# Kernel optimization log

Measured on AMD Instinct MI355X. Metric: run time of the kernel, lower is better.

Reference implementation:

```python
import jax, jax.numpy as jnp
import numpy as np

IN_FEATURES = 4096
OUT_FEATURES = 32000


def setup_inputs() -> dict:
    key = jax.random.key(0)
    kx, kw, ks, kb = jax.random.split(key, 4)
    x = jax.random.normal(kx, (16, 1, IN_FEATURES), dtype=jnp.float32)
    # int8 weight buffer, per torch.randint(-128, 127, ...)
    weight_int8 = jax.random.randint(kw, (OUT_FEATURES, IN_FEATURES), -128, 127, dtype=jnp.int8)
    scale = jax.random.uniform(ks, (OUT_FEATURES, 1), dtype=jnp.float32)
    bias = jax.random.uniform(kb, (1, OUT_FEATURES), dtype=jnp.float32)
    return {"x": x, "weight_int8": weight_int8, "scale": scale, "bias": bias}


def reference(x, weight_int8, scale, bias):
    # F.linear(x, W.type_as(x)): upcast int8 weight to activation dtype, then matmul
    w = weight_int8.astype(x.dtype)               # [O, I]
    out = jnp.einsum('bsi,oi->bso', x, w)         # [B, S, O]
    out = out * scale.T                           # per-output-channel scale, [1, O] broadcast
    out = out + bias                              # [1, O] broadcast
    return out.astype(x.dtype)
```

## Files before the change

kernel.cpp:

```cpp
#include <hip/hip_runtime.h>

#define IN_F  4096
#define OUT_F 32000
#define KC    128
#define NT    (IN_F / KC)

typedef __attribute__((ext_vector_type(8))) short bf16x8;
typedef __attribute__((ext_vector_type(4))) float f32x4;
typedef unsigned int u32;

__device__ __forceinline__ short bf(float f) {
    __bf16 h = (__bf16)f;
    short s;
    __builtin_memcpy(&s, &h, 2);
    return s;
}

__device__ __forceinline__ void gload16(const void* g, void* l) {
    __builtin_amdgcn_global_load_lds(
        (const __attribute__((address_space(1))) u32*)g,
        (__attribute__((address_space(3))) u32*)l, 16, 0, 0);
}

__device__ __forceinline__ int swzW(int r) {
    return ((r & 7) << 5) | (((r >> 3) & 1) << 4);
}

__global__ __launch_bounds__(256) void w8a16_kernel(
    const int* __restrict__ W, const float* __restrict__ X,
    const float* __restrict__ scale, const float* __restrict__ bias,
    float* __restrict__ out)
{
    __shared__ __align__(16) int   Wl[2][64][KC];
    __shared__ __align__(16) short Xl[2][16][KC];

    const int tid  = threadIdx.x;
    const int lane = tid & 63;
    const int wave = tid >> 6;
    const int n    = lane & 15;
    const int kg   = lane >> 4;
    const int lo   = lane & 31;
    const int hi   = lane >> 5;
    const int o_base = blockIdx.x * 64;

    float4 xreg[2];
    f32x4  acc = {0.f, 0.f, 0.f, 0.f};

    #define LOADX(t)                                                              \
        _Pragma("unroll")                                                         \
        for (int j = 0; j < 2; ++j) {                                             \
            const int r = wave * 4 + 2 * j + hi;                                  \
            xreg[j] = *reinterpret_cast<const float4*>(                           \
                X + (size_t)r * IN_F + (t) * KC + lo * 4);                        \
        }

    #define GLOADW(buf, t)                                                        \
        _Pragma("unroll")                                                         \
        for (int j = 0; j < 8; ++j) {                                             \
            const int r  = wave * 16 + 2 * j + hi;                                \
            const char* gp = (const char*)W                                       \
                + ((size_t)(o_base + r) * IN_F + (size_t)(t) * KC) * 4            \
                + ((lo * 16) ^ swzW(r));                                          \
            gload16(gp, &Wl[buf][wave * 16 + 2 * j][0]);                          \
        }

    #define XWRITE(buf)                                                           \
        _Pragma("unroll")                                                         \
        for (int j = 0; j < 2; ++j) {                                             \
            const int r = wave * 4 + 2 * j + hi;                                  \
            short4 v;                                                             \
            v.x = bf(xreg[j].x); v.y = bf(xreg[j].y);                             \
            v.z = bf(xreg[j].z); v.w = bf(xreg[j].w);                             \
            char* p = (char*)&Xl[buf][r][0] + ((lo * 8) ^ ((r & 7) << 4));        \
            *reinterpret_cast<short4*>(p) = v;                                    \
        }

    const int rA    = wave * 16 + n;
    const int swzA  = swzW(rA);
    const int swzAx = (n & 7) << 4;

    #define COMPUTE(buf)                                                          \
        _Pragma("unroll")                                                         \
        for (int s = 0; s < KC / 32; ++s) {                                       \
            const int o0 = (s * 128 + kg * 32) ^ swzA;                            \
            const int4 qa = *reinterpret_cast<const int4*>(                       \
                (const char*)&Wl[buf][rA][0] + o0);                               \
            const int4 qb = *reinterpret_cast<const int4*>(                       \
                (const char*)&Wl[buf][rA][0] + (o0 ^ 16));                        \
            bf16x8 a;                                                             \
            a[0]=bf((float)qa.x); a[1]=bf((float)qa.y);                           \
            a[2]=bf((float)qa.z); a[3]=bf((float)qa.w);                           \
            a[4]=bf((float)qb.x); a[5]=bf((float)qb.y);                           \
            a[6]=bf((float)qb.z); a[7]=bf((float)qb.w);                           \
            const int ox = (s * 64 + kg * 16) ^ swzAx;                            \
            bf16x8 b = *reinterpret_cast<const bf16x8*>(                          \
                (const char*)&Xl[buf][n][0] + ox);                                \
            acc = __builtin_amdgcn_mfma_f32_16x16x32_bf16(a, b, acc, 0, 0, 0);    \
        }

    LOADX(0);
    GLOADW(0, 0);
    XWRITE(0);
    __syncthreads();

    for (int t = 0; t < NT; ++t) {
        const int cur = t & 1;
        if (t + 1 < NT) {
            LOADX(t + 1);
            GLOADW(cur ^ 1, t + 1);
        }
        COMPUTE(cur);
        if (t + 1 < NT) { XWRITE(cur ^ 1); }
        __syncthreads();
    }

    const int o = o_base + wave * 16 + kg * 4;
    const float4 sc = *reinterpret_cast<const float4*>(scale + o);
    const float4 bs = *reinterpret_cast<const float4*>(bias + o);
    float4 rr;
    rr.x = acc[0] * sc.x + bs.x;
    rr.y = acc[1] * sc.y + bs.y;
    rr.z = acc[2] * sc.z + bs.z;
    rr.w = acc[3] * sc.w + bs.w;
    *reinterpret_cast<float4*>(out + (size_t)n * OUT_F + o) = rr;

    #undef LOADX
    #undef GLOADW
    #undef XWRITE
    #undef COMPUTE
}

extern "C" void kernel_launch(void* const* d_in, const int* in_sizes, int n_in,
                              void* d_out, int out_size, void* d_ws, size_t ws_size,
                              hipStream_t stream) {
    const float* x     = (const float*)d_in[0];
    const int*   w     = (const int*)  d_in[1];
    const float* scale = (const float*)d_in[2];
    const float* bias  = (const float*)d_in[3];
    float* out = (float*)d_out;
    (void)in_sizes; (void)n_in; (void)d_ws; (void)ws_size; (void)out_size;

    w8a16_kernel<<<dim3(OUT_F / 64), dim3(256), 0, stream>>>(w, x, scale, bias, out);
}
```

Baseline: 98.61 us.

## Drop X LDS staging and block barriers, pipeline loads with explicit vmcnt waits

X activations are now loaded straight into per-lane registers in MFMA B-operand order and converted to bf16 there, so the shared X buffer and its write pass go away. Each wave only reads the W rows it loaded itself, so the per-tile __syncthreads is replaced by explicit s_waitcnt vmcnt/lgkmcnt and sched_barrier. The next tile's loads are issued as soon as the current LDS buffer has been read into registers, which keeps two tiles of loads in flight. In exchange, every wave redundantly fetches X from cache and register pressure goes up. Correctness also depends on the hand-counted vmcnt thresholds matching the number of issued loads.

New measurement: 108.6 us. +10.1%, slower.

```diff
diff --git a/kernel.cpp b/kernel.cpp
--- a/kernel.cpp
+++ b/kernel.cpp
@@ -31,8 +31,7 @@
     const float* __restrict__ scale, const float* __restrict__ bias,
     float* __restrict__ out)
 {
-    __shared__ __align__(16) int   Wl[2][64][KC];
-    __shared__ __align__(16) short Xl[2][16][KC];
+    __shared__ __align__(16) int Wl[2][64][KC];
 
     const int tid  = threadIdx.x;
     const int lane = tid & 63;
@@ -43,76 +42,74 @@
     const int hi   = lane >> 5;
     const int o_base = blockIdx.x * 64;
 
-    float4 xreg[2];
+    float4 xrA[8], xrB[8];
     f32x4  acc = {0.f, 0.f, 0.f, 0.f};
 
-    #define LOADX(t)                                                              \
-        _Pragma("unroll")                                                         \
-        for (int j = 0; j < 2; ++j) {                                             \
-            const int r = wave * 4 + 2 * j + hi;                                  \
-            xreg[j] = *reinterpret_cast<const float4*>(                           \
-                X + (size_t)r * IN_F + (t) * KC + lo * 4);                        \
-        }
+    const int rA   = wave * 16 + n;
+    const int swzA = swzW(rA);
 
     #define GLOADW(buf, t)                                                        \
         _Pragma("unroll")                                                         \
         for (int j = 0; j < 8; ++j) {                                             \
-            const int r  = wave * 16 + 2 * j + hi;                                \
+            const int r = wave * 16 + 2 * j + hi;                                 \
             const char* gp = (const char*)W                                       \
                 + ((size_t)(o_base + r) * IN_F + (size_t)(t) * KC) * 4            \
                 + ((lo * 16) ^ swzW(r));                                          \
             gload16(gp, &Wl[buf][wave * 16 + 2 * j][0]);                          \
         }
 
-    #define XWRITE(buf)                                                           \
+    #define LOADX(XR, t)                                                          \
         _Pragma("unroll")                                                         \
-        for (int j = 0; j < 2; ++j) {                                             \
-            const int r = wave * 4 + 2 * j + hi;                                  \
-            short4 v;                                                             \
-            v.x = bf(xreg[j].x); v.y = bf(xreg[j].y);                             \
-            v.z = bf(xreg[j].z); v.w = bf(xreg[j].w);                             \
-            char* p = (char*)&Xl[buf][r][0] + ((lo * 8) ^ ((r & 7) << 4));        \
-            *reinterpret_cast<short4*>(p) = v;                                    \
+        for (int s = 0; s < 4; ++s) {                                             \
+            const float* xp = X + (size_t)n * IN_F + (t) * KC + s * 32 + kg * 8;  \
+            XR[2*s]   = *reinterpret_cast<const float4*>(xp);                     \
+            XR[2*s+1] = *reinterpret_cast<const float4*>(xp + 4);                 \
         }
 
-    const int rA    = wave * 16 + n;
-    const int swzA  = swzW(rA);
-    const int swzAx = (n & 7) << 4;
+    #define BODY(buf, XR, VMS, DOISS, tnext)                                      \
+    {                                                                             \
+        asm volatile("s_waitcnt vmcnt(" VMS ")" ::: "memory");                    \
+        __builtin_amdgcn_sched_barrier(0);                                        \
+        const char* wbase = (const char*)&Wl[buf][rA][0];                         \
+        int4 q[8];                                                                \
+        _Pragma("unroll")                                                         \
+        for (int s = 0; s < 4; ++s) {                                             \
+            const int o0 = (s * 128 + kg * 32) ^ swzA;                            \
+            q[2*s]   = *reinterpret_cast<const int4*>(wbase + o0);                \
+            q[2*s+1] = *reinterpret_cast<const int4*>(wbase + (o0 ^ 16));         \
+        }                                                                         \
+        bf16x8 B[4];                                                              \
+        _Pragma("unroll")                                                         \
+        for (int s = 0; s < 4; ++s) {                                             \
+            B[s][0]=bf(XR[2*s].x);   B[s][1]=bf(XR[2*s].y);                       \
+            B[s][2]=bf(XR[2*s].z);   B[s][3]=bf(XR[2*s].w);                       \
+            B[s][4]=bf(XR[2*s+1].x); B[s][5]=bf(XR[2*s+1].y);                     \
+            B[s][6]=bf(XR[2*s+1].z); B[s][7]=bf(XR[2*s+1].w);                     \
+        }                                                                         \
+        asm volatile("s_waitcnt lgkmcnt(0)" ::: "memory");                        \
+        __builtin_amdgcn_sched_barrier(0);                                        \
+        if (DOISS) { GLOADW(buf, tnext); LOADX(XR, tnext); }                      \
+        _Pragma("unroll")                                                         \
+        for (int s = 0; s < 4; ++s) {                                             \
+            bf16x8 a;                                                             \
+            a[0]=bf((float)q[2*s].x);   a[1]=bf((float)q[2*s].y);                 \
+            a[2]=bf((float)q[2*s].z);   a[3]=bf((float)q[2*s].w);                 \
+            a[4]=bf((float)q[2*s+1].x); a[5]=bf((float)q[2*s+1].y);               \
+            a[6]=bf((float)q[2*s+1].z); a[7]=bf((float)q[2*s+1].w);               \
+            acc = __builtin_amdgcn_mfma_f32_16x16x32_bf16(a, B[s], acc, 0, 0, 0); \
+        }                                                                         \
+    }
 
-    #define COMPUTE(buf)                                                          \
-        _Pragma("unroll")                                                         \
-        for (int s = 0; s < KC / 32; ++s) {                                       \
-            const int o0 = (s * 128 + kg * 32) ^ swzA;                            \
-            const int4 qa = *reinterpret_cast<const int4*>(                       \
-                (const char*)&Wl[buf][rA][0] + o0);                               \
-            const int4 qb = *reinterpret_cast<const int4*>(                       \
-                (const char*)&Wl[buf][rA][0] + (o0 ^ 16));                        \
-            bf16x8 a;                                                             \
-            a[0]=bf((float)qa.x); a[1]=bf((float)qa.y);                           \
-            a[2]=bf((float)qa.z); a[3]=bf((float)qa.w);                           \
-            a[4]=bf((float)qb.x); a[5]=bf((float)qb.y);                           \
-            a[6]=bf((float)qb.z); a[7]=bf((float)qb.w);                           \
-            const int ox = (s * 64 + kg * 16) ^ swzAx;                            \
-            bf16x8 b = *reinterpret_cast<const bf16x8*>(                          \
-                (const char*)&Xl[buf][n][0] + ox);                                \
-            acc = __builtin_amdgcn_mfma_f32_16x16x32_bf16(a, b, acc, 0, 0, 0);    \
-        }
+    GLOADW(0, 0); LOADX(xrA, 0);
+    __builtin_amdgcn_sched_barrier(0);
+    GLOADW(1, 1); LOADX(xrB, 1);
 
-    LOADX(0);
-    GLOADW(0, 0);
-    XWRITE(0);
-    __syncthreads();
-
-    for (int t = 0; t < NT; ++t) {
-        const int cur = t & 1;
-        if (t + 1 < NT) {
-            LOADX(t + 1);
-            GLOADW(cur ^ 1, t + 1);
-        }
-        COMPUTE(cur);
-        if (t + 1 < NT) { XWRITE(cur ^ 1); }
-        __syncthreads();
+    for (int t = 0; t < NT - 2; t += 2) {
+        BODY(0, xrA, "16", 1, t + 2);
+        BODY(1, xrB, "16", 1, t + 3);
     }
+    BODY(0, xrA, "16", 0, 0);
+    BODY(1, xrB, "0",  0, 0);
 
     const int o = o_base + wave * 16 + kg * 4;
     const float4 sc = *reinterpret_cast<const float4*>(scale + o);
@@ -124,10 +121,9 @@
     rr.w = acc[3] * sc.w + bs.w;
     *reinterpret_cast<float4*>(out + (size_t)n * OUT_F + o) = rr;
 
+    #undef GLOADW
     #undef LOADX
-    #undef GLOADW
-    #undef XWRITE
-    #undef COMPUTE
+    #undef BODY
 }
 
 extern "C" void kernel_launch(void* const* d_in, const int* in_sizes, int n_in,
```
